# Performance work log

Measured on AMD Instinct MI355X. Metric: run time of the kernel, lower is better.

## Reference

```python
import jax, jax.numpy as jnp
import numpy as np

EPS = 1e-5
K = 41  # hardcoded default of get_graph_feature


def _knn_idx(x, k):
    # x: [B, C, N]; pd[b,i,j] = -||x_i - x_j||^2 (larger = closer)
    xt = jnp.swapaxes(x, 1, 2)                       # [B, N, C]
    inner = -2.0 * jnp.einsum('bnc,bcm->bnm', xt, x)  # [B, N, N]
    xx = jnp.sum(x * x, axis=1)                      # [B, N]
    pd = -xx[:, None, :] - inner - xx[:, :, None]
    return jax.lax.top_k(pd, k)[1]                   # [B, N, k]


def _graph_feature(x, k):
    # x: [B, C, N] -> [B, 2C, N, k] = concat(neighbor_feat, center_feat)
    xt = jnp.swapaxes(x, 1, 2)                       # [B, N, C]
    idx = _knn_idx(x, k)                             # [B, N, k]
    neigh = jax.vmap(lambda pts, i: pts[i])(xt, idx)  # [B, N, k, C]
    center = jnp.broadcast_to(xt[:, :, None, :], neigh.shape)
    feat = jnp.concatenate([neigh, center], axis=-1)  # [B, N, k, 2C]
    return jnp.transpose(feat, (0, 3, 1, 2))


def _conv_bn_relu(x, w, g, b, m, v):
    # 1x1 conv (no bias) + eval-mode BatchNorm2d + ReLU, fused affine form
    y = jnp.einsum('oc,bcnk->bonk', w, x)
    inv = g / jnp.sqrt(v + EPS)
    scale = inv[None, :, None, None]
    shift = (b - m * inv)[None, :, None, None]
    return jax.nn.relu(y * scale + shift)


def setup_inputs() -> dict:
    key = jax.random.key(0)
    ks = jax.random.split(key, 32)
    B, N = 2, 4096
    chans = [(6, 64), (64, 64), (64, 128), (128, 256), (512, 256)]
    inp = {"x": jax.random.normal(ks[0], (B, 3, N), dtype=jnp.float32)}
    for i, (cin, cout) in enumerate(chans, start=1):
        inp[f"w{i}"] = jax.random.normal(ks[i], (cout, cin), dtype=jnp.float32) * np.float32(np.sqrt(2.0 / cin))
        inp[f"g{i}"] = 1.0 + 0.1 * jax.random.normal(ks[5 + i], (cout,), dtype=jnp.float32)
        inp[f"b{i}"] = 0.1 * jax.random.normal(ks[10 + i], (cout,), dtype=jnp.float32)
        inp[f"m{i}"] = 0.1 * jax.random.normal(ks[15 + i], (cout,), dtype=jnp.float32)
        inp[f"v{i}"] = jax.random.uniform(ks[20 + i], (cout,), dtype=jnp.float32, minval=0.5, maxval=1.5)
    return inp


def reference(x, w1, g1, b1, m1, v1, w2, g2, b2, m2, v2, w3, g3, b3, m3, v3,
              w4, g4, b4, m4, v4, w5, g5, b5, m5, v5):
    feat = _graph_feature(x, K)                      # [B, 6, N, k]
    h = _conv_bn_relu(feat, w1, g1, b1, m1, v1)      # [B, 64, N, k]
    x1 = jnp.max(h, axis=-1, keepdims=True)
    h = _conv_bn_relu(h, w2, g2, b2, m2, v2)         # [B, 64, N, k]
    x2 = jnp.max(h, axis=-1, keepdims=True)
    h = _conv_bn_relu(h, w3, g3, b3, m3, v3)         # [B, 128, N, k]
    x3 = jnp.max(h, axis=-1, keepdims=True)
    h = _conv_bn_relu(h, w4, g4, b4, m4, v4)         # [B, 256, N, k]
    x4 = jnp.max(h, axis=-1, keepdims=True)
    cat = jnp.concatenate([x1, x2, x3, x4], axis=1)  # [B, 512, N, 1]
    out = _conv_bn_relu(cat, w5, g5, b5, m5, v5)[..., 0]  # [B, 256, N]
    return out, feat
```

## Files before the change

kernel.cpp:

```cpp
#include <hip/hip_runtime.h>
#include <math.h>

#define NP 4096
#define NB 2
#define KNN 41
#define KPAD 48
#define PPW 4
#define NBLK 3
#define NPTS_TOT (NB*NP)
#define HUP 132

#define WS_W1T 0
#define WS_SH1 384
#define WS_W2T 448
#define WS_SH2 4544
#define WS_W3T 4608
#define WS_SH3 12800
#define WS_W4T 12928
#define WS_SH4 45696
#define WS_W5F 45952
#define WS_SH5 177024
#define WS_IDX_BYTES (177280*4)

__global__ __launch_bounds__(256) void prep_weights(
    const float* __restrict__ w1, const float* __restrict__ g1, const float* __restrict__ b1,
    const float* __restrict__ m1, const float* __restrict__ v1,
    const float* __restrict__ w2, const float* __restrict__ g2, const float* __restrict__ b2,
    const float* __restrict__ m2, const float* __restrict__ v2,
    const float* __restrict__ w3, const float* __restrict__ g3, const float* __restrict__ b3,
    const float* __restrict__ m3, const float* __restrict__ v3,
    const float* __restrict__ w4, const float* __restrict__ g4, const float* __restrict__ b4,
    const float* __restrict__ m4, const float* __restrict__ v4,
    const float* __restrict__ w5, const float* __restrict__ g5, const float* __restrict__ b5,
    const float* __restrict__ m5, const float* __restrict__ v5,
    float* __restrict__ wsf)
{
  const int wg = blockIdx.x;
  const int t  = threadIdx.x;
  if (wg == 0) {
    if (t < 64) {
      const float i1 = g1[t] / sqrtf(v1[t] + 1e-5f);
      wsf[WS_SH1 + t] = b1[t] - m1[t]*i1;
#pragma unroll
      for (int ci = 0; ci < 6; ++ci) wsf[WS_W1T + ci*64 + t] = w1[t*6 + ci] * i1;
      const float i2 = g2[t] / sqrtf(v2[t] + 1e-5f);
      wsf[WS_SH2 + t] = b2[t] - m2[t]*i2;
    }
    if (t < 128) {
      const float i3 = g3[t] / sqrtf(v3[t] + 1e-5f);
      wsf[WS_SH3 + t] = b3[t] - m3[t]*i3;
    }
    {
      const float i4 = g4[t] / sqrtf(v4[t] + 1e-5f);
      wsf[WS_SH4 + t] = b4[t] - m4[t]*i4;
      const float i5 = g5[t] / sqrtf(v5[t] + 1e-5f);
      wsf[WS_SH5 + t] = b5[t] - m5[t]*i5;
    }
  } else if (wg == 1) {
    for (int e = t; e < 4096; e += 256) {
      const int ci = e >> 6, co = e & 63;
      const float inv = g2[co] / sqrtf(v2[co] + 1e-5f);
      wsf[WS_W2T + e] = w2[co*64 + ci] * inv;
    }
  } else if (wg == 2) {
    for (int e = t; e < 8192; e += 256) {
      const int ci = e >> 7, co = e & 127;
      const float inv = g3[co] / sqrtf(v3[co] + 1e-5f);
      wsf[WS_W3T + e] = w3[co*64 + ci] * inv;
    }
  } else if (wg <= 4) {
    const int base = (wg - 3) * 16384;
    for (int k = t; k < 16384; k += 256) {
      const int e = base + k;
      const int ci = e >> 8, co = e & 255;
      const float inv = g4[co] / sqrtf(v4[co] + 1e-5f);
      wsf[WS_W4T + e] = w4[co*128 + ci] * inv;
    }
  } else {
    const int base = (wg - 5) * 4096;
    for (int k = t; k < 4096; k += 256) {
      const int e = base + k;
      const int co = e >> 9, q = e & 511;
      const float inv = g5[co] / sqrtf(v5[co] + 1e-5f);
      wsf[WS_W5F + e] = w5[co*512 + q] * inv;
    }
  }
}

__global__ __launch_bounds__(512) void knn_feat_kernel(
    const float* __restrict__ x,
    float* __restrict__ feat_out,
    int* __restrict__ idx_ws)
{
  __shared__ float xs0[NP];
  __shared__ float xs1[NP];
  __shared__ float xs2[NP];
  __shared__ int idxbuf[8][KNN];
  __shared__ int flagbuf[8];

  const int tid  = threadIdx.x;
  const int wave = tid >> 6;
  const int lane = tid & 63;
  const int row0 = blockIdx.x * 8;
  const int b    = row0 >> 12;
  const float* xb = x + b * 3 * NP;

  for (int t = tid; t < NP; t += 512) {
    xs0[t] = xb[t];
    xs1[t] = xb[NP + t];
    xs2[t] = xb[2*NP + t];
  }
  if (lane == 0) flagbuf[wave] = 0;
  __syncthreads();

  const int i = (row0 & (NP-1)) + wave;
  const float a0 = xs0[i], a1 = xs1[i], a2 = xs2[i];
  const float xxi = (a0*a0 + a1*a1) + a2*a2;

  float lv[12]; int lj[12];
#pragma unroll
  for (int u = 0; u < 12; ++u) { lv[u] = -__builtin_inff(); lj[u] = -1; }

  for (int t = 0; t < NP/64; ++t) {
    const int j = t*64 + lane;
    const float b0 = xs0[j], b1 = xs1[j], b2 = xs2[j];
    const float dot  = fmaf(a2, b2, fmaf(a1, b1, a0*b0));
    const float xxj  = (b0*b0 + b1*b1) + b2*b2;
    const float inner = -2.0f * dot;
    const float pd   = ((0.0f - xxj) - inner) - xxi;
    float cv = pd; int cj = j;
#pragma unroll
    for (int u = 0; u < 12; ++u) {
      const bool gt = (cv > lv[u]);
      const float tv = gt ? lv[u] : cv;
      const int   tj = gt ? lj[u] : cj;
      lv[u] = gt ? cv : lv[u];
      lj[u] = gt ? cj : lj[u];
      cv = tv; cj = tj;
    }
  }

  int pops = 0;
  for (int m = 0; m < KNN; ++m) {
    float vv = lv[0]; int jj = lj[0];
#pragma unroll
    for (int s = 1; s < 64; s <<= 1) {
      const float ov = __shfl_xor(vv, s);
      const int   oj = __shfl_xor(jj, s);
      const bool take = (ov > vv) || ((ov == vv) && ((unsigned)oj < (unsigned)jj));
      vv = take ? ov : vv;
      jj = take ? oj : jj;
    }
    if (lane == 0) idxbuf[wave][m] = jj;
    if (lj[0] == jj) {
#pragma unroll
      for (int u = 0; u < 11; ++u) { lv[u] = lv[u+1]; lj[u] = lj[u+1]; }
      lv[11] = -__builtin_inff(); lj[11] = -1;
      ++pops;
      if (pops == 12 && m < KNN-1) flagbuf[wave] = 1;
    }
  }

  if (flagbuf[wave] != 0 && lane == 0) {
    float fv[KNN]; int fj[KNN];
    for (int u = 0; u < KNN; ++u) { fv[u] = -__builtin_inff(); fj[u] = -1; }
    for (int j = 0; j < NP; ++j) {
      const float b0 = xs0[j], b1 = xs1[j], b2 = xs2[j];
      const float dot = fmaf(a2, b2, fmaf(a1, b1, a0*b0));
      const float xxj = (b0*b0 + b1*b1) + b2*b2;
      const float pd  = ((0.0f - xxj) - (-2.0f*dot)) - xxi;
      if (pd > fv[KNN-1]) {
        int p = KNN-1;
        while (p > 0 && fv[p-1] < pd) { fv[p] = fv[p-1]; fj[p] = fj[p-1]; --p; }
        fv[p] = pd; fj[p] = j;
      }
    }
    for (int m = 0; m < KNN; ++m) idxbuf[wave][m] = fj[m];
  }

  if (lane < KNN) {
    const int j = idxbuf[wave][lane];
    idx_ws[(row0 + wave) * KNN + lane] = j;
    const int fo = b * 6 * NP * KNN;
    feat_out[fo + (0*NP + i)*KNN + lane] = xs0[j];
    feat_out[fo + (1*NP + i)*KNN + lane] = xs1[j];
    feat_out[fo + (2*NP + i)*KNN + lane] = xs2[j];
    feat_out[fo + (3*NP + i)*KNN + lane] = xs0[i];
    feat_out[fo + (4*NP + i)*KNN + lane] = xs1[i];
    feat_out[fo + (5*NP + i)*KNN + lane] = xs2[i];
  }
}

__device__ __forceinline__ void kmax16(float y, int l, int* slot) {
  float r = y;
  r = fmaxf(r, __shfl_down(r, 8, 16));
  r = fmaxf(r, __shfl_down(r, 4, 16));
  r = fmaxf(r, __shfl_down(r, 2, 16));
  r = fmaxf(r, __shfl_down(r, 1, 16));
  if ((l & 15) == 0) atomicMax(slot, __float_as_int(r));
}

__global__ __launch_bounds__(512, 6) void fused_conv_kernel(
    const float* __restrict__ x,
    const int* __restrict__ idx_ws,
    const float* __restrict__ wsf,
    float* __restrict__ out)
{
  __shared__ float hu[64][HUP];
  __shared__ int   xbuf[PPW][512];

  const int tid = threadIdx.x;
  const int w   = __builtin_amdgcn_readfirstlane(tid >> 6);
  const int l   = tid & 63;
  const int pt0 = blockIdx.x * PPW;

  for (int t = tid; t < PPW*512; t += 512) ((int*)xbuf)[t] = 0;

  for (int blk = 0; blk < NBLK; ++blk) {
    const int s  = blk*64 + l;
    const int lp = s / KPAD;
    const int kk = s - lp*KPAD;
    const int pt = pt0 + lp;
    const int bb = pt >> 12;
    const int n  = pt & (NP-1);

    const int j = (kk < KNN) ? idx_ws[pt*KNN + kk] : n;
    const float f0 = x[(bb*3+0)*NP + j];
    const float f1 = x[(bb*3+1)*NP + j];
    const float f2 = x[(bb*3+2)*NP + j];
    const float f3 = x[(bb*3+0)*NP + n];
    const float f4 = x[(bb*3+1)*NP + n];
    const float f5 = x[(bb*3+2)*NP + n];
    __syncthreads();

    {
      float acc[8];
#pragma unroll
      for (int cc = 0; cc < 8; ++cc) acc[cc] = 0.0f;
      const float f[6] = {f0, f1, f2, f3, f4, f5};
#pragma unroll
      for (int ci = 0; ci < 6; ++ci) {
        const float* wr = wsf + WS_W1T + ci*64 + w*8;
#pragma unroll
        for (int cc = 0; cc < 8; ++cc) acc[cc] = fmaf(wr[cc], f[ci], acc[cc]);
      }
      const float* sh = wsf + WS_SH1 + w*8;
      float y[8];
#pragma unroll
      for (int cc = 0; cc < 8; ++cc) y[cc] = fmaxf(acc[cc] + sh[cc], 0.0f);
      *(float4*)&hu[l][w*8]     = make_float4(y[0], y[1], y[2], y[3]);
      *(float4*)&hu[l][w*8 + 4] = make_float4(y[4], y[5], y[6], y[7]);
#pragma unroll
      for (int cc = 0; cc < 8; ++cc) kmax16(y[cc], l, &xbuf[lp][w*8 + cc]);
    }
    __syncthreads();

    {
      float acc[8];
#pragma unroll
      for (int cc = 0; cc < 8; ++cc) acc[cc] = 0.0f;
#pragma unroll 2
      for (int q = 0; q < 16; ++q) {
        const float4 av = *(const float4*)&hu[l][q*4];
        const float* w0 = wsf + WS_W2T + (q*4+0)*64 + w*8;
        const float* w1 = wsf + WS_W2T + (q*4+1)*64 + w*8;
        const float* w2r = wsf + WS_W2T + (q*4+2)*64 + w*8;
        const float* w3r = wsf + WS_W2T + (q*4+3)*64 + w*8;
#pragma unroll
        for (int cc = 0; cc < 8; ++cc) acc[cc] = fmaf(w0[cc], av.x, acc[cc]);
#pragma unroll
        for (int cc = 0; cc < 8; ++cc) acc[cc] = fmaf(w1[cc], av.y, acc[cc]);
#pragma unroll
        for (int cc = 0; cc < 8; ++cc) acc[cc] = fmaf(w2r[cc], av.z, acc[cc]);
#pragma unroll
        for (int cc = 0; cc < 8; ++cc) acc[cc] = fmaf(w3r[cc], av.w, acc[cc]);
      }
      const float* sh = wsf + WS_SH2 + w*8;
      float y[8];
#pragma unroll
      for (int cc = 0; cc < 8; ++cc) y[cc] = fmaxf(acc[cc] + sh[cc], 0.0f);
      *(float4*)&hu[l][64 + w*8]     = make_float4(y[0], y[1], y[2], y[3]);
      *(float4*)&hu[l][64 + w*8 + 4] = make_float4(y[4], y[5], y[6], y[7]);
#pragma unroll
      for (int cc = 0; cc < 8; ++cc) kmax16(y[cc], l, &xbuf[lp][64 + w*8 + cc]);
    }
    __syncthreads();

    {
      float acc[16];
#pragma unroll
      for (int cc = 0; cc < 16; ++cc) acc[cc] = 0.0f;
#pragma unroll 2
      for (int q = 0; q < 16; ++q) {
        const float4 av = *(const float4*)&hu[l][64 + q*4];
        const float* w0 = wsf + WS_W3T + (q*4+0)*128 + w*16;
        const float* w1 = wsf + WS_W3T + (q*4+1)*128 + w*16;
        const float* w2r = wsf + WS_W3T + (q*4+2)*128 + w*16;
        const float* w3r = wsf + WS_W3T + (q*4+3)*128 + w*16;
#pragma unroll
        for (int cc = 0; cc < 16; ++cc) acc[cc] = fmaf(w0[cc], av.x, acc[cc]);
#pragma unroll
        for (int cc = 0; cc < 16; ++cc) acc[cc] = fmaf(w1[cc], av.y, acc[cc]);
#pragma unroll
        for (int cc = 0; cc < 16; ++cc) acc[cc] = fmaf(w2r[cc], av.z, acc[cc]);
#pragma unroll
        for (int cc = 0; cc < 16; ++cc) acc[cc] = fmaf(w3r[cc], av.w, acc[cc]);
      }
      __syncthreads();
      const float* sh = wsf + WS_SH3 + w*16;
      float y[16];
#pragma unroll
      for (int cc = 0; cc < 16; ++cc) y[cc] = fmaxf(acc[cc] + sh[cc], 0.0f);
#pragma unroll
      for (int qq = 0; qq < 4; ++qq)
        *(float4*)&hu[l][w*16 + qq*4] = make_float4(y[qq*4], y[qq*4+1], y[qq*4+2], y[qq*4+3]);
#pragma unroll
      for (int cc = 0; cc < 16; ++cc) kmax16(y[cc], l, &xbuf[lp][128 + w*16 + cc]);
    }
    __syncthreads();

    {
      float acc[32];
#pragma unroll
      for (int cc = 0; cc < 32; ++cc) acc[cc] = 0.0f;
#pragma unroll 2
      for (int q = 0; q < 32; ++q) {
        const float4 av = *(const float4*)&hu[l][q*4];
        const float* w0 = wsf + WS_W4T + (q*4+0)*256 + w*32;
        const float* w1 = wsf + WS_W4T + (q*4+1)*256 + w*32;
        const float* w2r = wsf + WS_W4T + (q*4+2)*256 + w*32;
        const float* w3r = wsf + WS_W4T + (q*4+3)*256 + w*32;
#pragma unroll
        for (int cc = 0; cc < 32; ++cc) acc[cc] = fmaf(w0[cc], av.x, acc[cc]);
#pragma unroll
        for (int cc = 0; cc < 32; ++cc) acc[cc] = fmaf(w1[cc], av.y, acc[cc]);
#pragma unroll
        for (int cc = 0; cc < 32; ++cc) acc[cc] = fmaf(w2r[cc], av.z, acc[cc]);
#pragma unroll
        for (int cc = 0; cc < 32; ++cc) acc[cc] = fmaf(w3r[cc], av.w, acc[cc]);
      }
      const float* sh = wsf + WS_SH4 + w*32;
#pragma unroll
      for (int cc = 0; cc < 32; ++cc) {
        const float y = fmaxf(acc[cc] + sh[cc], 0.0f);
        kmax16(y, l, &xbuf[lp][256 + w*32 + cc]);
      }
    }
  }
  __syncthreads();

  {
    const int co = tid & 255;
    const int pr = tid >> 8;
    float a0 = 0.f, a1 = 0.f;
    const float4* wr  = (const float4*)(wsf + WS_W5F + co*512);
    const float4* xb0 = (const float4*)&xbuf[pr*2    ][0];
    const float4* xb1 = (const float4*)&xbuf[pr*2 + 1][0];
#pragma unroll 4
    for (int q = 0; q < 128; ++q) {
      const float4 wv = wr[q];
      const float4 x0 = xb0[q];
      const float4 x1 = xb1[q];
      a0 = fmaf(wv.x, x0.x, a0); a0 = fmaf(wv.y, x0.y, a0);
      a0 = fmaf(wv.z, x0.z, a0); a0 = fmaf(wv.w, x0.w, a0);
      a1 = fmaf(wv.x, x1.x, a1); a1 = fmaf(wv.y, x1.y, a1);
      a1 = fmaf(wv.z, x1.z, a1); a1 = fmaf(wv.w, x1.w, a1);
    }
    const float sh5 = wsf[WS_SH5 + co];
    float2 res;
    res.x = fmaxf(a0 + sh5, 0.0f);
    res.y = fmaxf(a1 + sh5, 0.0f);
    const int bb = pt0 >> 12;
    const int n0 = (pt0 & (NP-1)) + pr*2;
    *(float2*)&out[(bb*256 + co)*NP + n0] = res;
  }
}

extern "C" void kernel_launch(void* const* d_in, const int* in_sizes, int n_in,
                              void* d_out, int out_size, void* d_ws, size_t ws_size,
                              hipStream_t stream) {
  (void)in_sizes; (void)n_in; (void)out_size; (void)ws_size;
  const float* x = (const float*)d_in[0];
  const float* W[5], *G[5], *Bb[5], *M[5], *V[5];
  for (int i = 0; i < 5; ++i) {
    W[i]  = (const float*)d_in[1 + 5*i + 0];
    G[i]  = (const float*)d_in[1 + 5*i + 1];
    Bb[i] = (const float*)d_in[1 + 5*i + 2];
    M[i]  = (const float*)d_in[1 + 5*i + 3];
    V[i]  = (const float*)d_in[1 + 5*i + 4];
  }
  float* out = (float*)d_out;
  float* feat_out = out + NB*256*NP;
  float* wsf = (float*)d_ws;
  int* idx_ws = (int*)((char*)d_ws + WS_IDX_BYTES);

  prep_weights<<<37, 256, 0, stream>>>(
      W[0], G[0], Bb[0], M[0], V[0],
      W[1], G[1], Bb[1], M[1], V[1],
      W[2], G[2], Bb[2], M[2], V[2],
      W[3], G[3], Bb[3], M[3], V[3],
      W[4], G[4], Bb[4], M[4], V[4],
      wsf);

  knn_feat_kernel<<<NPTS_TOT/8, 512, 0, stream>>>(x, feat_out, idx_ws);

  fused_conv_kernel<<<NPTS_TOT/PPW, 512, 0, stream>>>(x, idx_ws, wsf, out);
}
```

Measured before the change: 775.0 us.

## Remap neighbor slots per lane and accumulate layer-4 max in registers

Changes the mapping so each 16-lane group owns one point and each block iteration covers 16 neighbors, instead of a padded 48-slot layout spread across lanes. Neighbor coordinates are gathered once by wave 0 into shared memory and center coordinates are loaded once. The layer-4 max is kept in 32 registers across iterations and reduced with atomics only once at the end, cutting shuffle and atomic traffic. The cost is more register pressure and an extra shared buffer with a sync dependency.

```diff
diff --git a/kernel.cpp b/kernel.cpp
--- a/kernel.cpp
+++ b/kernel.cpp
@@ -4,7 +4,6 @@
 #define NP 4096
 #define NB 2
 #define KNN 41
-#define KPAD 48
 #define PPW 4
 #define NBLK 3
 #define NPTS_TOT (NB*NP)
@@ -206,38 +205,44 @@
     const float* __restrict__ wsf,
     float* __restrict__ out)
 {
+  __shared__ float featb[3][64];
   __shared__ float hu[64][HUP];
   __shared__ int   xbuf[PPW][512];
 
   const int tid = threadIdx.x;
   const int w   = __builtin_amdgcn_readfirstlane(tid >> 6);
   const int l   = tid & 63;
-  const int pt0 = blockIdx.x * PPW;
+  const int lp  = l >> 4;
+  const int pt  = blockIdx.x * PPW + lp;
+  const int bb  = pt >> 12;
+  const int n   = pt & (NP-1);
 
   for (int t = tid; t < PPW*512; t += 512) ((int*)xbuf)[t] = 0;
 
+  const float c0 = x[(bb*3+0)*NP + n];
+  const float c1 = x[(bb*3+1)*NP + n];
+  const float c2 = x[(bb*3+2)*NP + n];
+
+  float s4max[32];
+#pragma unroll
+  for (int cc = 0; cc < 32; ++cc) s4max[cc] = 0.0f;
+
   for (int blk = 0; blk < NBLK; ++blk) {
-    const int s  = blk*64 + l;
-    const int lp = s / KPAD;
-    const int kk = s - lp*KPAD;
-    const int pt = pt0 + lp;
-    const int bb = pt >> 12;
-    const int n  = pt & (NP-1);
-
-    const int j = (kk < KNN) ? idx_ws[pt*KNN + kk] : n;
-    const float f0 = x[(bb*3+0)*NP + j];
-    const float f1 = x[(bb*3+1)*NP + j];
-    const float f2 = x[(bb*3+2)*NP + j];
-    const float f3 = x[(bb*3+0)*NP + n];
-    const float f4 = x[(bb*3+1)*NP + n];
-    const float f5 = x[(bb*3+2)*NP + n];
+    const int kk = blk*16 + (l & 15);
+
+    if (w == 0) {
+      const int j = (kk < KNN) ? idx_ws[pt*KNN + kk] : n;
+      featb[0][l] = x[(bb*3+0)*NP + j];
+      featb[1][l] = x[(bb*3+1)*NP + j];
+      featb[2][l] = x[(bb*3+2)*NP + j];
+    }
     __syncthreads();
 
     {
+      const float f[6] = {featb[0][l], featb[1][l], featb[2][l], c0, c1, c2};
       float acc[8];
 #pragma unroll
       for (int cc = 0; cc < 8; ++cc) acc[cc] = 0.0f;
-      const float f[6] = {f0, f1, f2, f3, f4, f5};
 #pragma unroll
       for (int ci = 0; ci < 6; ++ci) {
         const float* wr = wsf + WS_W1T + ci*64 + w*8;
@@ -341,12 +346,13 @@
       }
       const float* sh = wsf + WS_SH4 + w*32;
 #pragma unroll
-      for (int cc = 0; cc < 32; ++cc) {
-        const float y = fmaxf(acc[cc] + sh[cc], 0.0f);
-        kmax16(y, l, &xbuf[lp][256 + w*32 + cc]);
-      }
-    }
-  }
+      for (int cc = 0; cc < 32; ++cc)
+        s4max[cc] = fmaxf(s4max[cc], fmaxf(acc[cc] + sh[cc], 0.0f));
+    }
+  }
+
+#pragma unroll
+  for (int cc = 0; cc < 32; ++cc) kmax16(s4max[cc], l, &xbuf[lp][256 + w*32 + cc]);
   __syncthreads();
 
   {
@@ -370,9 +376,9 @@
     float2 res;
     res.x = fmaxf(a0 + sh5, 0.0f);
     res.y = fmaxf(a1 + sh5, 0.0f);
-    const int bb = pt0 >> 12;
-    const int n0 = (pt0 & (NP-1)) + pr*2;
-    *(float2*)&out[(bb*256 + co)*NP + n0] = res;
+    const int bbs = blockIdx.x * PPW >> 12;
+    const int n0 = ((blockIdx.x * PPW) & (NP-1)) + pr*2;
+    *(float2*)&out[(bbs*256 + co)*NP + n0] = res;
   }
 }
 
```

After: 799.1 us. 3.1% more time.
